# Performance work log

Hardware: AMD Instinct MI355X
Metric: run time of the kernel (lower is better)

The kernel has to match this reference:

```python
import jax, jax.numpy as jnp
import numpy as np

N = 2097152
RES = 512
N_LEVELS = 6  # 512,256,128,64,32,16 (stop at LIGHT_MIN_RES=16)
MIN_ROUGHNESS = 0.08
MAX_ROUGHNESS = 0.5


def _dot(a, b):
    return jnp.sum(a * b, axis=-1, keepdims=True)


def _safe_normalize(x):
    return x / jnp.sqrt(jnp.clip(_dot(x, x), 1e-20, None))


def _reflect(x, n):
    return 2.0 * _dot(x, n) * n - x


def _rgb_to_srgb(x):
    return jnp.where(x <= 0.0031308, 12.92 * x,
                     1.055 * jnp.power(jnp.maximum(x, 0.0031308), 1.0 / 2.4) - 0.055)


def _cube_face_uv(d):
    # OpenGL / nvdiffrast cube-map convention (inverse of util.cube_to_dir)
    x, y, z = d[..., 0], d[..., 1], d[..., 2]
    ax, ay, az = jnp.abs(x), jnp.abs(y), jnp.abs(z)
    is_x = (ax >= ay) & (ax >= az)
    is_y = (~is_x) & (ay >= az)
    face = jnp.where(is_x, jnp.where(x > 0, 0, 1),
           jnp.where(is_y, jnp.where(y > 0, 2, 3),
                           jnp.where(z > 0, 4, 5)))
    ma = jnp.maximum(jnp.where(is_x, ax, jnp.where(is_y, ay, az)), 1e-20)
    u = jnp.where(is_x, jnp.where(x > 0, -z, z),
        jnp.where(is_y, x, jnp.where(z > 0, x, -x)))
    v = jnp.where(is_y, jnp.where(y > 0, z, -z), -y)
    return face, u / ma, v / ma


def _bilinear_gather(tex, face, fx, fy):
    # tex: [6,H,W,C]; face/fx/fy: [N]
    H, W = tex.shape[1], tex.shape[2]
    x0 = jnp.floor(fx); y0 = jnp.floor(fy)
    tx = (fx - x0)[:, None]; ty = (fy - y0)[:, None]
    x0i = jnp.clip(x0.astype(jnp.int32), 0, W - 1)
    x1i = jnp.clip(x0i + 1, 0, W - 1)
    y0i = jnp.clip(y0.astype(jnp.int32), 0, H - 1)
    y1i = jnp.clip(y0i + 1, 0, H - 1)
    c00 = tex[face, y0i, x0i]; c01 = tex[face, y0i, x1i]
    c10 = tex[face, y1i, x0i]; c11 = tex[face, y1i, x1i]
    return (c00 * (1 - tx) + c01 * tx) * (1 - ty) + (c10 * (1 - tx) + c11 * tx) * ty


def _sample_cubemap(tex, dirs):
    H, W = tex.shape[1], tex.shape[2]
    face, u, v = _cube_face_uv(dirs)
    return _bilinear_gather(tex, face, (u * 0.5 + 0.5) * W - 0.5, (v * 0.5 + 0.5) * H - 0.5)


def _sample_cubemap_mip(mips, dirs, level):
    # trilinear: bilinear in each of the two bracketing mip levels + lerp on level
    L = len(mips)
    samples = jnp.stack([_sample_cubemap(m, dirs) for m in mips], axis=0)  # [L,N,C]
    lvl = jnp.clip(level, 0.0, L - 1.0)
    l0 = jnp.floor(lvl).astype(jnp.int32)
    l1 = jnp.minimum(l0 + 1, L - 1)
    f = (lvl - l0.astype(lvl.dtype))[:, None]
    n = jnp.arange(dirs.shape[0])
    return samples[l0, n] * (1 - f) + samples[l1, n] * f


def _sample_lut(lut, uv):
    # lut: [H,W,C]; uv in [0,1], u -> width, v -> height, clamp boundary
    H, W = lut.shape[0], lut.shape[1]
    fx = uv[:, 0] * W - 0.5; fy = uv[:, 1] * H - 0.5
    x0 = jnp.floor(fx); y0 = jnp.floor(fy)
    tx = (fx - x0)[:, None]; ty = (fy - y0)[:, None]
    x0i = jnp.clip(x0.astype(jnp.int32), 0, W - 1); x1i = jnp.clip(x0i + 1, 0, W - 1)
    y0i = jnp.clip(y0.astype(jnp.int32), 0, H - 1); y1i = jnp.clip(y0i + 1, 0, H - 1)
    c00 = lut[y0i, x0i]; c01 = lut[y0i, x1i]; c10 = lut[y1i, x0i]; c11 = lut[y1i, x1i]
    return (c00 * (1 - tx) + c01 * tx) * (1 - ty) + (c10 * (1 - tx) + c11 * tx) * ty


def _get_mip(roughness, n_levels):
    lo = (jnp.clip(roughness, MIN_ROUGHNESS, MAX_ROUGHNESS) - MIN_ROUGHNESS) \
         / (MAX_ROUGHNESS - MIN_ROUGHNESS) * (n_levels - 2)
    hi = (jnp.clip(roughness, MAX_ROUGHNESS, 1.0) - MAX_ROUGHNESS) / (1.0 - MAX_ROUGHNESS) + n_levels - 2
    return jnp.where(roughness < MAX_ROUGHNESS, lo, hi)


def _shade(view_dir, normal, kd, ks, reflect_occ, diffuse_map, mips, fg_lut):
    roughness = ks[:, 1:2]
    metallic = ks[:, 2:3]
    spec_col = (1.0 - metallic) * 0.04 + kd * metallic
    diff_col = kd * (1.0 - metallic)
    reflvec = _safe_normalize(_reflect(view_dir, normal))
    diffuse = jnp.clip(_sample_cubemap(diffuse_map, normal), 0.0, None)
    shaded = diffuse * diff_col * (1.0 - ks[:, 0:1])
    NdotV = jnp.clip(_dot(view_dir, normal), 1e-4, None)
    fg = _sample_lut(fg_lut, jnp.concatenate([NdotV, roughness], axis=-1))
    miplevel = _get_mip(roughness[:, 0], len(mips))
    spec = jnp.clip(_sample_cubemap_mip(mips, reflvec, miplevel), 0.0, None)
    reflectance = spec_col * fg[:, 0:1] + fg[:, 1:2]
    shaded = shaded + spec * reflectance * (1.0 - reflect_occ)
    return _rgb_to_srgb(jnp.clip(shaded, 0.0, 1.0))


def setup_inputs() -> dict:
    key = jax.random.key(0)
    k = jax.random.split(key, 16)
    inp = {
        "view_dir": _safe_normalize(jax.random.normal(k[0], (N, 3), jnp.float32)),
        "normal": _safe_normalize(jax.random.normal(k[1], (N, 3), jnp.float32)),
        "kd": jax.random.uniform(k[2], (N, 3), jnp.float32),
        "ks": jax.random.uniform(k[3], (N, 3), jnp.float32),
        "reflect_occ": jax.random.uniform(k[4], (N, 1), jnp.float32),
    }
    # learned / prefiltered environment light parameters (from build_mips)
    inp["diffuse_map"] = jax.random.uniform(k[5], (6, 16, 16, 3), jnp.float32)
    res = RES
    for i in range(N_LEVELS):
        inp[f"spec{i}"] = jax.random.uniform(k[6 + i], (6, res, res, 3), jnp.float32)
        res //= 2
    inp["fg_lut"] = jax.random.uniform(k[12], (256, 256, 2), jnp.float32)
    return inp


def reference(view_dir, normal, kd, ks, reflect_occ, diffuse_map,
              spec0, spec1, spec2, spec3, spec4, spec5, fg_lut):
    mips = [spec0, spec1, spec2, spec3, spec4, spec5]
    return _shade(view_dir, normal, kd, ks, reflect_occ, diffuse_map, mips, fg_lut)
```

## Files before the change

kernel.cpp:

```cpp
#include <hip/hip_runtime.h>
#include <hip/hip_fp16.h>
#include <math.h>


typedef unsigned int u32;

__device__ __forceinline__ u32 enc9e5(float r, float g, float b) {
    r = fminf(fmaxf(r, 0.f), 65408.f);
    g = fminf(fmaxf(g, 0.f), 65408.f);
    b = fminf(fmaxf(b, 0.f), 65408.f);
    float maxc = fmaxf(r, fmaxf(g, b));
    int e = ((__float_as_int(maxc) >> 23) & 0xff) - 127;
    int exp_p = max(e + 16, 0);
    float denom = __int_as_float((exp_p + 103) << 23);
    int maxm = (int)(maxc / denom + 0.5f);
    if (maxm == 512) { exp_p += 1; denom *= 2.f; }
    float rd = 1.f / denom;
    u32 rm = (u32)(r * rd + 0.5f);
    u32 gm = (u32)(g * rd + 0.5f);
    u32 bm = (u32)(b * rd + 0.5f);
    return rm | (gm << 9) | (bm << 18) | ((u32)exp_p << 27);
}

__device__ __forceinline__ void dec9e5_acc(u32 pk, float w, float& r, float& g, float& b) {
    float scale = __int_as_float((int)(((pk >> 27) & 31u) + 103u) << 23) * w;
    r += (float)(pk & 511u) * scale;
    g += (float)((pk >> 9) & 511u) * scale;
    b += (float)((pk >> 18) & 511u) * scale;
}

struct CubeQ { int idx; float w00, w01, w10, w11; };

__device__ __forceinline__ CubeQ cube_addr_q(int lr, float dx, float dy, float dz) {
    float ax = fabsf(dx), ay = fabsf(dy), az = fabsf(dz);
    bool is_x = (ax >= ay) && (ax >= az);
    bool is_y = (!is_x) && (ay >= az);
    int face = is_x ? (dx > 0.f ? 0 : 1)
                    : (is_y ? (dy > 0.f ? 2 : 3) : (dz > 0.f ? 4 : 5));
    float ma = fmaxf(is_x ? ax : (is_y ? ay : az), 1e-20f);
    float u = is_x ? (dx > 0.f ? -dz : dz) : (is_y ? dx : (dz > 0.f ? dx : -dx));
    float v = is_y ? (dy > 0.f ? dz : -dz) : -dy;
    float inv = __builtin_amdgcn_rcpf(ma);
    float R = (float)(1 << lr);
    float fx = (u * inv * 0.5f + 0.5f) * R - 0.5f;
    float fy = (v * inv * 0.5f + 0.5f) * R - 0.5f;
    float x0f = floorf(fx), y0f = floorf(fy);
    float tx = fx - x0f, ty = fy - y0f;
    int W = 1 << lr;
    int x0 = min(max((int)x0f, 0), W - 1);
    int y0 = min(max((int)y0f, 0), W - 1);
    CubeQ a;
    a.idx = (face << (2 * lr)) + (y0 << lr) + x0;
    a.w00 = (1.f - tx) * (1.f - ty);
    a.w01 = tx * (1.f - ty);
    a.w10 = (1.f - tx) * ty;
    a.w11 = tx * ty;
    return a;
}

__device__ __forceinline__ void gather_q9(uint4 q, const CubeQ& a,
                                          float& r, float& g, float& b) {
    r = 0.f; g = 0.f; b = 0.f;
    dec9e5_acc(q.x, a.w00, r, g, b);
    dec9e5_acc(q.y, a.w01, r, g, b);
    dec9e5_acc(q.z, a.w10, r, g, b);
    dec9e5_acc(q.w, a.w11, r, g, b);
}

__device__ __forceinline__ float srgb1(float x) {
    float p = 1.055f * __builtin_amdgcn_exp2f(
                  __builtin_amdgcn_logf(fmaxf(x, 0.0031308f)) * (1.0f / 2.4f)) - 0.055f;
    return (x <= 0.0031308f) ? (12.92f * x) : p;
}

#define SPEC_TOTAL 2096640
#define DIF_OFF    SPEC_TOTAL
#define LUT_OFF    (SPEC_TOTAL + 1536)
#define ALL_QUADS  (SPEC_TOTAL + 1536 + 65536)

__global__ __launch_bounds__(256)
void repack_all(const float* __restrict__ s0, const float* __restrict__ s1,
                const float* __restrict__ s2, const float* __restrict__ s3,
                const float* __restrict__ s4, const float* __restrict__ s5,
                const float* __restrict__ diffuse_map,
                const float2* __restrict__ lut,
                uint4* __restrict__ dst)
{
    int i = blockIdx.x * blockDim.x + threadIdx.x;
    if (i >= ALL_QUADS) return;

    if (i >= LUT_OFF) {
        int k = i - LUT_OFF;
        int y = k >> 8, x = k & 255;
        int x1 = min(x + 1, 255), y1 = min(y + 1, 255);
        float2 c00 = lut[(y << 8) + x],  c01 = lut[(y << 8) + x1];
        float2 c10 = lut[(y1 << 8) + x], c11 = lut[(y1 << 8) + x1];
        __half2 h00 = __floats2half2_rn(c00.x, c00.y);
        __half2 h01 = __floats2half2_rn(c01.x, c01.y);
        __half2 h10 = __floats2half2_rn(c10.x, c10.y);
        __half2 h11 = __floats2half2_rn(c11.x, c11.y);
        uint4 q;
        q.x = *reinterpret_cast<u32*>(&h00);
        q.y = *reinterpret_cast<u32*>(&h01);
        q.z = *reinterpret_cast<u32*>(&h10);
        q.w = *reinterpret_cast<u32*>(&h11);
        dst[i] = q;
        return;
    }

    const float* src;
    int lr, local;
    if (i >= DIF_OFF)       { src = diffuse_map; lr = 4; local = i - DIF_OFF; }
    else if (i < 1572864)   { src = s0; lr = 9; local = i; }
    else if (i < 1966080)   { src = s1; lr = 8; local = i - 1572864; }
    else if (i < 2064384)   { src = s2; lr = 7; local = i - 1966080; }
    else if (i < 2088960)   { src = s3; lr = 6; local = i - 2064384; }
    else if (i < 2095104)   { src = s4; lr = 5; local = i - 2088960; }
    else                    { src = s5; lr = 4; local = i - 2095104; }

    int W = 1 << lr;
    int face = local >> (2 * lr);
    int rem = local & (W * W - 1);
    int y = rem >> lr, x = rem & (W - 1);
    int x1 = min(x + 1, W - 1), y1 = min(y + 1, W - 1);
    int base = face << (2 * lr);
    int i00 = 3 * (base + (y << lr) + x);
    int i01 = 3 * (base + (y << lr) + x1);
    int i10 = 3 * (base + (y1 << lr) + x);
    int i11 = 3 * (base + (y1 << lr) + x1);
    uint4 q;
    q.x = enc9e5(src[i00], src[i00 + 1], src[i00 + 2]);
    q.y = enc9e5(src[i01], src[i01 + 1], src[i01 + 2]);
    q.z = enc9e5(src[i10], src[i10 + 1], src[i10 + 2]);
    q.w = enc9e5(src[i11], src[i11 + 1], src[i11 + 2]);
    dst[i] = q;
}

struct MipSel { const uint4* tA; const uint4* tB; float f; };

__device__ __forceinline__ MipSel mip_select(const uint4* __restrict__ q, float rough) {
    const float MINR = 0.08f, MAXR = 0.5f;
    float lo = (fminf(fmaxf(rough, MINR), MAXR) - MINR) * (4.0f / (MAXR - MINR));
    float hi = (fminf(fmaxf(rough, MAXR), 1.0f) - MAXR) * (1.0f / (1.0f - MAXR)) + 4.0f;
    float lvl = (rough < MAXR) ? lo : hi;
    lvl = fminf(fmaxf(lvl, 0.f), 5.f);
    int l0 = min(max((int)floorf(lvl), 0), 5);
    int l1 = min(l0 + 1, 5);
    static const int OFF[6] = {0, 1572864, 1966080, 2064384, 2088960, 2095104};
    MipSel s;
    s.tA = q + OFF[l0];
    s.tB = q + OFF[l1];
    s.f = lvl - (float)l0;
    return s;
}

__global__ __launch_bounds__(256)
void envlight_quad4(const float4* __restrict__ vd4,
                    const float4* __restrict__ nm4,
                    const float4* __restrict__ kd4,
                    const float4* __restrict__ ks4,
                    const float4* __restrict__ oc4,
                    const uint4* __restrict__ q,
                    float4* __restrict__ out4, int n4)
{
    int t = blockIdx.x * blockDim.x + threadIdx.x;
    if (t >= n4) return;

    float vf[12], nf[12], kf[12], qf[12], of[12];
    *(float4*)&vf[0] = vd4[3 * t];     *(float4*)&vf[4] = vd4[3 * t + 1];  *(float4*)&vf[8] = vd4[3 * t + 2];
    *(float4*)&nf[0] = nm4[3 * t];     *(float4*)&nf[4] = nm4[3 * t + 1];  *(float4*)&nf[8] = nm4[3 * t + 2];
    *(float4*)&kf[0] = kd4[3 * t];     *(float4*)&kf[4] = kd4[3 * t + 1];  *(float4*)&kf[8] = kd4[3 * t + 2];
    *(float4*)&qf[0] = ks4[3 * t];     *(float4*)&qf[4] = ks4[3 * t + 1];  *(float4*)&qf[8] = ks4[3 * t + 2];
    float4 occ4 = oc4[t];
    float occv[4] = {occ4.x, occ4.y, occ4.z, occ4.w};

    const uint4* dquad = q + DIF_OFF;
    const uint4* lutq  = q + LUT_OFF;

    CubeQ aA[4], aB[4], aD[4];
    int lutI[4];
    float lw00[4], lw01[4], lw10[4], lw11[4];
    float fmip[4], vdotn_[4];
    const uint4 *pA[4], *pB[4];

    #pragma unroll
    for (int p = 0; p < 4; ++p) {
        float vx = vf[3 * p], vy = vf[3 * p + 1], vz = vf[3 * p + 2];
        float nx = nf[3 * p], ny = nf[3 * p + 1], nz = nf[3 * p + 2];
        float rough = qf[3 * p + 1];

        float vdotn = vx * nx + vy * ny + vz * nz;
        vdotn_[p] = vdotn;
        float rx = 2.f * vdotn * nx - vx;
        float ry = 2.f * vdotn * ny - vy;
        float rz = 2.f * vdotn * nz - vz;
        float rlen2 = fmaxf(rx * rx + ry * ry + rz * rz, 1e-20f);
        float rinv = __builtin_amdgcn_rsqf(rlen2);
        rx *= rinv; ry *= rinv; rz *= rinv;

        aD[p] = cube_addr_q(4, nx, ny, nz);

        float NdotV = fmaxf(vdotn, 1e-4f);
        float fx = NdotV * 256.f - 0.5f;
        float fy = rough * 256.f - 0.5f;
        float x0f = floorf(fx), y0f = floorf(fy);
        float tx = fx - x0f, ty = fy - y0f;
        int x0 = min(max((int)x0f, 0), 255);
        int y0 = min(max((int)y0f, 0), 255);
        lutI[p] = (y0 << 8) + x0;
        lw00[p] = (1.f - tx) * (1.f - ty);
        lw01[p] = tx * (1.f - ty);
        lw10[p] = (1.f - tx) * ty;
        lw11[p] = tx * ty;

        MipSel ms = mip_select(q, rough);
        fmip[p] = ms.f;
        pA[p] = ms.tA; pB[p] = ms.tB;
        const float MINR = 0.08f, MAXR = 0.5f;
        float lo = (fminf(fmaxf(rough, MINR), MAXR) - MINR) * (4.0f / (MAXR - MINR));
        float hi = (fminf(fmaxf(rough, MAXR), 1.0f) - MAXR) * (1.0f / (1.0f - MAXR)) + 4.0f;
        float lvl = (rough < MAXR) ? lo : hi;
        lvl = fminf(fmaxf(lvl, 0.f), 5.f);
        int l0 = min(max((int)floorf(lvl), 0), 5);
        int l1 = min(l0 + 1, 5);
        aA[p] = cube_addr_q(9 - l0, rx, ry, rz);
        aB[p] = cube_addr_q(9 - l1, rx, ry, rz);
    }

    uint4 qA[4], qB[4], lq[4], dq[4];
    #pragma unroll
    for (int p = 0; p < 4; ++p) {
        qA[p] = pA[p][aA[p].idx];
        qB[p] = pB[p][aB[p].idx];
        lq[p] = lutq[lutI[p]];
        dq[p] = dquad[aD[p].idx];
    }

    #pragma unroll
    for (int p = 0; p < 4; ++p) {
        float kdx = kf[3 * p], kdy = kf[3 * p + 1], kdz = kf[3 * p + 2];
        float ks0 = qf[3 * p], metallic = qf[3 * p + 2];

        float ar, ag, ab_, br, bg, bb;
        gather_q9(qA[p], aA[p], ar, ag, ab_);
        gather_q9(qB[p], aB[p], br, bg, bb);

        __half2 h00 = *reinterpret_cast<__half2*>(&lq[p].x);
        __half2 h01 = *reinterpret_cast<__half2*>(&lq[p].y);
        __half2 h10 = *reinterpret_cast<__half2*>(&lq[p].z);
        __half2 h11 = *reinterpret_cast<__half2*>(&lq[p].w);
        float2 c00 = __half22float2(h00), c01 = __half22float2(h01);
        float2 c10 = __half22float2(h10), c11 = __half22float2(h11);
        float fg0 = c00.x * lw00[p] + c01.x * lw01[p] + c10.x * lw10[p] + c11.x * lw11[p];
        float fg1 = c00.y * lw00[p] + c01.y * lw01[p] + c10.y * lw10[p] + c11.y * lw11[p];

        float dfr, dfg, dfb;
        gather_q9(dq[p], aD[p], dfr, dfg, dfb);
        dfr = fmaxf(dfr, 0.f); dfg = fmaxf(dfg, 0.f); dfb = fmaxf(dfb, 0.f);

        float f = fmip[p];
        float spr = fmaxf(ar * (1.f - f) + br * f, 0.f);
        float spg = fmaxf(ag * (1.f - f) + bg * f, 0.f);
        float spb = fmaxf(ab_ * (1.f - f) + bb * f, 0.f);

        float m = metallic;
        float scx = (1.f - m) * 0.04f + kdx * m;
        float scy = (1.f - m) * 0.04f + kdy * m;
        float scz = (1.f - m) * 0.04f + kdz * m;
        float dcx = kdx * (1.f - m);
        float dcy = kdy * (1.f - m);
        float dcz = kdz * (1.f - m);

        float kds = 1.f - ks0;
        float shx = dfr * dcx * kds;
        float shy = dfg * dcy * kds;
        float shz = dfb * dcz * kds;

        float om = 1.f - occv[p];
        shx += spr * (scx * fg0 + fg1) * om;
        shy += spg * (scy * fg0 + fg1) * om;
        shz += spb * (scz * fg0 + fg1) * om;

        of[3 * p + 0] = srgb1(fminf(fmaxf(shx, 0.f), 1.f));
        of[3 * p + 1] = srgb1(fminf(fmaxf(shy, 0.f), 1.f));
        of[3 * p + 2] = srgb1(fminf(fmaxf(shz, 0.f), 1.f));
    }

    out4[3 * t]     = *(float4*)&of[0];
    out4[3 * t + 1] = *(float4*)&of[4];
    out4[3 * t + 2] = *(float4*)&of[8];
}

__global__ __launch_bounds__(256)
void envlight_quad1(const float* __restrict__ view_dir,
                    const float* __restrict__ normal,
                    const float* __restrict__ kd,
                    const float* __restrict__ ks,
                    const float* __restrict__ reflect_occ,
                    const uint4* __restrict__ q,
                    float* __restrict__ out, int base, int n)
{
    int i = base + blockIdx.x * blockDim.x + threadIdx.x;
    if (i >= n) return;

    const uint4* dquad = q + DIF_OFF;
    const uint4* lutq  = q + LUT_OFF;

    float vx = view_dir[3 * i + 0], vy = view_dir[3 * i + 1], vz = view_dir[3 * i + 2];
    float nx = normal[3 * i + 0],  ny = normal[3 * i + 1],  nz = normal[3 * i + 2];
    float kdx = kd[3 * i + 0], kdy = kd[3 * i + 1], kdz = kd[3 * i + 2];
    float ks0 = ks[3 * i + 0], rough = ks[3 * i + 1], metallic = ks[3 * i + 2];
    float occ = reflect_occ[i];

    float vdotn = vx * nx + vy * ny + vz * nz;
    float rx = 2.f * vdotn * nx - vx;
    float ry = 2.f * vdotn * ny - vy;
    float rz = 2.f * vdotn * nz - vz;
    float rlen2 = fmaxf(rx * rx + ry * ry + rz * rz, 1e-20f);
    float rinv = __builtin_amdgcn_rsqf(rlen2);
    rx *= rinv; ry *= rinv; rz *= rinv;

    CubeQ aD = cube_addr_q(4, nx, ny, nz);

    float NdotV = fmaxf(vdotn, 1e-4f);
    float fx = NdotV * 256.f - 0.5f;
    float fy = rough * 256.f - 0.5f;
    float x0f = floorf(fx), y0f = floorf(fy);
    float tx = fx - x0f, ty = fy - y0f;
    int x0 = min(max((int)x0f, 0), 255);
    int y0 = min(max((int)y0f, 0), 255);
    int lutI = (y0 << 8) + x0;
    float lw00 = (1.f - tx) * (1.f - ty);
    float lw01 = tx * (1.f - ty);
    float lw10 = (1.f - tx) * ty;
    float lw11 = tx * ty;

    const float MINR = 0.08f, MAXR = 0.5f;
    float lo = (fminf(fmaxf(rough, MINR), MAXR) - MINR) * (4.0f / (MAXR - MINR));
    float hi = (fminf(fmaxf(rough, MAXR), 1.0f) - MAXR) * (1.0f / (1.0f - MAXR)) + 4.0f;
    float lvl = (rough < MAXR) ? lo : hi;
    lvl = fminf(fmaxf(lvl, 0.f), 5.f);
    int l0 = min(max((int)floorf(lvl), 0), 5);
    int l1 = min(l0 + 1, 5);
    float f = lvl - (float)l0;
    static const int OFF[6] = {0, 1572864, 1966080, 2064384, 2088960, 2095104};
    const uint4* tA = q + OFF[l0];
    const uint4* tB = q + OFF[l1];
    CubeQ aA = cube_addr_q(9 - l0, rx, ry, rz);
    CubeQ aB = cube_addr_q(9 - l1, rx, ry, rz);

    uint4 qA = tA[aA.idx];
    uint4 qB = tB[aB.idx];
    uint4 lq = lutq[lutI];
    uint4 dq = dquad[aD.idx];

    float ar, ag, ab_, br, bg, bb;
    gather_q9(qA, aA, ar, ag, ab_);
    gather_q9(qB, aB, br, bg, bb);

    __half2 h00 = *reinterpret_cast<__half2*>(&lq.x);
    __half2 h01 = *reinterpret_cast<__half2*>(&lq.y);
    __half2 h10 = *reinterpret_cast<__half2*>(&lq.z);
    __half2 h11 = *reinterpret_cast<__half2*>(&lq.w);
    float2 c00 = __half22float2(h00), c01 = __half22float2(h01);
    float2 c10 = __half22float2(h10), c11 = __half22float2(h11);
    float fg0 = c00.x * lw00 + c01.x * lw01 + c10.x * lw10 + c11.x * lw11;
    float fg1 = c00.y * lw00 + c01.y * lw01 + c10.y * lw10 + c11.y * lw11;

    float dfr, dfg, dfb;
    gather_q9(dq, aD, dfr, dfg, dfb);
    dfr = fmaxf(dfr, 0.f); dfg = fmaxf(dfg, 0.f); dfb = fmaxf(dfb, 0.f);

    float spr = fmaxf(ar * (1.f - f) + br * f, 0.f);
    float spg = fmaxf(ag * (1.f - f) + bg * f, 0.f);
    float spb = fmaxf(ab_ * (1.f - f) + bb * f, 0.f);

    float m = metallic;
    float scx = (1.f - m) * 0.04f + kdx * m;
    float scy = (1.f - m) * 0.04f + kdy * m;
    float scz = (1.f - m) * 0.04f + kdz * m;
    float dcx = kdx * (1.f - m);
    float dcy = kdy * (1.f - m);
    float dcz = kdz * (1.f - m);

    float kds = 1.f - ks0;
    float shx = dfr * dcx * kds;
    float shy = dfg * dcy * kds;
    float shz = dfb * dcz * kds;

    float om = 1.f - occ;
    shx += spr * (scx * fg0 + fg1) * om;
    shy += spg * (scy * fg0 + fg1) * om;
    shz += spb * (scz * fg0 + fg1) * om;

    out[3 * i + 0] = srgb1(fminf(fmaxf(shx, 0.f), 1.f));
    out[3 * i + 1] = srgb1(fminf(fmaxf(shy, 0.f), 1.f));
    out[3 * i + 2] = srgb1(fminf(fmaxf(shz, 0.f), 1.f));
}

extern "C" void kernel_launch(void* const* d_in, const int* in_sizes, int n_in,
                              void* d_out, int out_size, void* d_ws, size_t ws_size,
                              hipStream_t stream) {
    const float* view_dir    = (const float*)d_in[0];
    const float* normal      = (const float*)d_in[1];
    const float* kd          = (const float*)d_in[2];
    const float* ks          = (const float*)d_in[3];
    const float* reflect_occ = (const float*)d_in[4];
    const float* diffuse_map = (const float*)d_in[5];
    const float* s0          = (const float*)d_in[6];
    const float* s1          = (const float*)d_in[7];
    const float* s2          = (const float*)d_in[8];
    const float* s3          = (const float*)d_in[9];
    const float* s4          = (const float*)d_in[10];
    const float* s5          = (const float*)d_in[11];
    const float* fg_lut      = (const float*)d_in[12];
    float* out = (float*)d_out;

    int n = in_sizes[0] / 3;
    const size_t NEED_Q = (size_t)ALL_QUADS * 16;

    if (ws_size >= NEED_Q) {
        uint4* q = (uint4*)d_ws;
        repack_all<<<(ALL_QUADS + 255) / 256, 256, 0, stream>>>(
            s0, s1, s2, s3, s4, s5, diffuse_map, (const float2*)fg_lut, q);

        int n4 = n / 4;
        if (n4 > 0) {
            envlight_quad4<<<(n4 + 255) / 256, 256, 0, stream>>>(
                (const float4*)view_dir, (const float4*)normal,
                (const float4*)kd, (const float4*)ks,
                (const float4*)reflect_occ, q, (float4*)out, n4);
        }
        int tail = n - 4 * n4;
        if (tail > 0) {
            envlight_quad1<<<1, 256, 0, stream>>>(
                view_dir, normal, kd, ks, reflect_occ, q, out, 4 * n4, n);
        }
    } else {
        int n4 = n / 4;
        envlight_quad4<<<(n4 + 255) / 256, 256, 0, stream>>>(
            (const float4*)view_dir, (const float4*)normal,
            (const float4*)kd, (const float4*)ks,
            (const float4*)reflect_occ, (const uint4*)d_ws, (float4*)out, n4);
    }
}
```

Baseline: 226.6 us.

## Replace 4-pixel-per-thread shading kernel with one-pixel-per-thread kernel

Drops the float4-vectorised kernel that shaded four pixels per thread and uses a scalar kernel that shades one pixel per thread, with launch bounds asking for 8 blocks per SM. The second mip level's coordinates are now derived from the first level's by halving instead of rerunning the cube face projection. The aim is lower register pressure and higher occupancy so more gathers are in flight, at the cost of losing 16-byte vector loads and stores on the streaming inputs. A fallback kernel that samples the raw float textures is added for when the workspace is too small, fixing the old path that read an unfilled workspace.

Result: slower. 235.9 us (+4.1%).

```diff
diff --git a/kernel.cpp b/kernel.cpp
--- a/kernel.cpp
+++ b/kernel.cpp
@@ -29,48 +29,38 @@
     b += (float)((pk >> 18) & 511u) * scale;
 }
 
-struct CubeQ { int idx; float w00, w01, w10, w11; };
-
-__device__ __forceinline__ CubeQ cube_addr_q(int lr, float dx, float dy, float dz) {
-    float ax = fabsf(dx), ay = fabsf(dy), az = fabsf(dz);
-    bool is_x = (ax >= ay) && (ax >= az);
-    bool is_y = (!is_x) && (ay >= az);
-    int face = is_x ? (dx > 0.f ? 0 : 1)
-                    : (is_y ? (dy > 0.f ? 2 : 3) : (dz > 0.f ? 4 : 5));
-    float ma = fmaxf(is_x ? ax : (is_y ? ay : az), 1e-20f);
-    float u = is_x ? (dx > 0.f ? -dz : dz) : (is_y ? dx : (dz > 0.f ? dx : -dx));
-    float v = is_y ? (dy > 0.f ? dz : -dz) : -dy;
-    float inv = __builtin_amdgcn_rcpf(ma);
-    float R = (float)(1 << lr);
-    float fx = (u * inv * 0.5f + 0.5f) * R - 0.5f;
-    float fy = (v * inv * 0.5f + 0.5f) * R - 0.5f;
-    float x0f = floorf(fx), y0f = floorf(fy);
-    float tx = fx - x0f, ty = fy - y0f;
-    int W = 1 << lr;
-    int x0 = min(max((int)x0f, 0), W - 1);
-    int y0 = min(max((int)y0f, 0), W - 1);
-    CubeQ a;
-    a.idx = (face << (2 * lr)) + (y0 << lr) + x0;
-    a.w00 = (1.f - tx) * (1.f - ty);
-    a.w01 = tx * (1.f - ty);
-    a.w10 = (1.f - tx) * ty;
-    a.w11 = tx * ty;
-    return a;
-}
-
-__device__ __forceinline__ void gather_q9(uint4 q, const CubeQ& a,
+__device__ __forceinline__ void gather_q9(uint4 q, float tx, float ty,
                                           float& r, float& g, float& b) {
+    float w01 = tx * (1.f - ty);
+    float w00 = (1.f - tx) * (1.f - ty);
+    float w10 = (1.f - tx) * ty;
+    float w11 = tx * ty;
     r = 0.f; g = 0.f; b = 0.f;
-    dec9e5_acc(q.x, a.w00, r, g, b);
-    dec9e5_acc(q.y, a.w01, r, g, b);
-    dec9e5_acc(q.z, a.w10, r, g, b);
-    dec9e5_acc(q.w, a.w11, r, g, b);
+    dec9e5_acc(q.x, w00, r, g, b);
+    dec9e5_acc(q.y, w01, r, g, b);
+    dec9e5_acc(q.z, w10, r, g, b);
+    dec9e5_acc(q.w, w11, r, g, b);
 }
 
 __device__ __forceinline__ float srgb1(float x) {
     float p = 1.055f * __builtin_amdgcn_exp2f(
                   __builtin_amdgcn_logf(fmaxf(x, 0.0031308f)) * (1.0f / 2.4f)) - 0.055f;
     return (x <= 0.0031308f) ? (12.92f * x) : p;
+}
+
+__device__ __forceinline__ void cube_face_uv(float dx, float dy, float dz,
+                                             int& face, float& u, float& v) {
+    float ax = fabsf(dx), ay = fabsf(dy), az = fabsf(dz);
+    bool is_x = (ax >= ay) && (ax >= az);
+    bool is_y = (!is_x) && (ay >= az);
+    face = is_x ? (dx > 0.f ? 0 : 1)
+                : (is_y ? (dy > 0.f ? 2 : 3) : (dz > 0.f ? 4 : 5));
+    float ma = fmaxf(is_x ? ax : (is_y ? ay : az), 1e-20f);
+    float uu = is_x ? (dx > 0.f ? -dz : dz) : (is_y ? dx : (dz > 0.f ? dx : -dx));
+    float vv = is_y ? (dy > 0.f ? dz : -dz) : -dy;
+    float inv = __builtin_amdgcn_rcpf(ma);
+    u = uu * inv;
+    v = vv * inv;
 }
 
 #define SPEC_TOTAL 2096640
@@ -136,9 +126,55 @@
     dst[i] = q;
 }
 
-struct MipSel { const uint4* tA; const uint4* tB; float f; };
-
-__device__ __forceinline__ MipSel mip_select(const uint4* __restrict__ q, float rough) {
+__global__ __launch_bounds__(256, 8)
+void envlight_q1(const float* __restrict__ view_dir,
+                 const float* __restrict__ normal,
+                 const float* __restrict__ kd,
+                 const float* __restrict__ ks,
+                 const float* __restrict__ reflect_occ,
+                 const uint4* __restrict__ q,
+                 float* __restrict__ out, int n)
+{
+    int i = blockIdx.x * blockDim.x + threadIdx.x;
+    if (i >= n) return;
+
+    float vx = view_dir[3 * i + 0], vy = view_dir[3 * i + 1], vz = view_dir[3 * i + 2];
+    float nx = normal[3 * i + 0],  ny = normal[3 * i + 1],  nz = normal[3 * i + 2];
+    float rough = ks[3 * i + 1];
+
+    float vdotn = vx * nx + vy * ny + vz * nz;
+    float rx = 2.f * vdotn * nx - vx;
+    float ry = 2.f * vdotn * ny - vy;
+    float rz = 2.f * vdotn * nz - vz;
+    float rlen2 = fmaxf(rx * rx + ry * ry + rz * rz, 1e-20f);
+    float rinv = __builtin_amdgcn_rsqf(rlen2);
+    rx *= rinv; ry *= rinv; rz *= rinv;
+
+    float dtx, dty; int dIdx;
+    {
+        int face; float u, v;
+        cube_face_uv(nx, ny, nz, face, u, v);
+        float fx = (u * 0.5f + 0.5f) * 16.f - 0.5f;
+        float fy = (v * 0.5f + 0.5f) * 16.f - 0.5f;
+        float x0f = floorf(fx), y0f = floorf(fy);
+        dtx = fx - x0f; dty = fy - y0f;
+        int x0 = min(max((int)x0f, 0), 15);
+        int y0 = min(max((int)y0f, 0), 15);
+        dIdx = (face << 8) + (y0 << 4) + x0;
+    }
+
+    float ltx, lty; int lutI;
+    {
+        float NdotV = fmaxf(vdotn, 1e-4f);
+        float fx = NdotV * 256.f - 0.5f;
+        float fy = rough * 256.f - 0.5f;
+        float x0f = floorf(fx), y0f = floorf(fy);
+        ltx = fx - x0f; lty = fy - y0f;
+        int x0 = min(max((int)x0f, 0), 255);
+        int y0 = min(max((int)y0f, 0), 255);
+        lutI = (y0 << 8) + x0;
+    }
+
     const float MINR = 0.08f, MAXR = 0.5f;
     float lo = (fminf(fmaxf(rough, MINR), MAXR) - MINR) * (4.0f / (MAXR - MINR));
     float hi = (fminf(fmaxf(rough, MAXR), 1.0f) - MAXR) * (1.0f / (1.0f - MAXR)) + 4.0f;
@@ -146,217 +182,50 @@
     lvl = fminf(fmaxf(lvl, 0.f), 5.f);
     int l0 = min(max((int)floorf(lvl), 0), 5);
     int l1 = min(l0 + 1, 5);
-    static const int OFF[6] = {0, 1572864, 1966080, 2064384, 2088960, 2095104};
-    MipSel s;
-    s.tA = q + OFF[l0];
-    s.tB = q + OFF[l1];
-    s.f = lvl - (float)l0;
-    return s;
-}
-
-__global__ __launch_bounds__(256)
-void envlight_quad4(const float4* __restrict__ vd4,
-                    const float4* __restrict__ nm4,
-                    const float4* __restrict__ kd4,
-                    const float4* __restrict__ ks4,
-                    const float4* __restrict__ oc4,
-                    const uint4* __restrict__ q,
-                    float4* __restrict__ out4, int n4)
-{
-    int t = blockIdx.x * blockDim.x + threadIdx.x;
-    if (t >= n4) return;
-
-    float vf[12], nf[12], kf[12], qf[12], of[12];
-    *(float4*)&vf[0] = vd4[3 * t];     *(float4*)&vf[4] = vd4[3 * t + 1];  *(float4*)&vf[8] = vd4[3 * t + 2];
-    *(float4*)&nf[0] = nm4[3 * t];     *(float4*)&nf[4] = nm4[3 * t + 1];  *(float4*)&nf[8] = nm4[3 * t + 2];
-    *(float4*)&kf[0] = kd4[3 * t];     *(float4*)&kf[4] = kd4[3 * t + 1];  *(float4*)&kf[8] = kd4[3 * t + 2];
-    *(float4*)&qf[0] = ks4[3 * t];     *(float4*)&qf[4] = ks4[3 * t + 1];  *(float4*)&qf[8] = ks4[3 * t + 2];
-    float4 occ4 = oc4[t];
-    float occv[4] = {occ4.x, occ4.y, occ4.z, occ4.w};
-
-    const uint4* dquad = q + DIF_OFF;
-    const uint4* lutq  = q + LUT_OFF;
-
-    CubeQ aA[4], aB[4], aD[4];
-    int lutI[4];
-    float lw00[4], lw01[4], lw10[4], lw11[4];
-    float fmip[4], vdotn_[4];
-    const uint4 *pA[4], *pB[4];
-
-    #pragma unroll
-    for (int p = 0; p < 4; ++p) {
-        float vx = vf[3 * p], vy = vf[3 * p + 1], vz = vf[3 * p + 2];
-        float nx = nf[3 * p], ny = nf[3 * p + 1], nz = nf[3 * p + 2];
-        float rough = qf[3 * p + 1];
-
-        float vdotn = vx * nx + vy * ny + vz * nz;
-        vdotn_[p] = vdotn;
-        float rx = 2.f * vdotn * nx - vx;
-        float ry = 2.f * vdotn * ny - vy;
-        float rz = 2.f * vdotn * nz - vz;
-        float rlen2 = fmaxf(rx * rx + ry * ry + rz * rz, 1e-20f);
-        float rinv = __builtin_amdgcn_rsqf(rlen2);
-        rx *= rinv; ry *= rinv; rz *= rinv;
-
-        aD[p] = cube_addr_q(4, nx, ny, nz);
-
-        float NdotV = fmaxf(vdotn, 1e-4f);
-        float fx = NdotV * 256.f - 0.5f;
-        float fy = rough * 256.f - 0.5f;
-        float x0f = floorf(fx), y0f = floorf(fy);
-        float tx = fx - x0f, ty = fy - y0f;
-        int x0 = min(max((int)x0f, 0), 255);
-        int y0 = min(max((int)y0f, 0), 255);
-        lutI[p] = (y0 << 8) + x0;
-        lw00[p] = (1.f - tx) * (1.f - ty);
-        lw01[p] = tx * (1.f - ty);
-        lw10[p] = (1.f - tx) * ty;
-        lw11[p] = tx * ty;
-
-        MipSel ms = mip_select(q, rough);
-        fmip[p] = ms.f;
-        pA[p] = ms.tA; pB[p] = ms.tB;
-        const float MINR = 0.08f, MAXR = 0.5f;
-        float lo = (fminf(fmaxf(rough, MINR), MAXR) - MINR) * (4.0f / (MAXR - MINR));
-        float hi = (fminf(fmaxf(rough, MAXR), 1.0f) - MAXR) * (1.0f / (1.0f - MAXR)) + 4.0f;
-        float lvl = (rough < MAXR) ? lo : hi;
-        lvl = fminf(fmaxf(lvl, 0.f), 5.f);
-        int l0 = min(max((int)floorf(lvl), 0), 5);
-        int l1 = min(l0 + 1, 5);
-        aA[p] = cube_addr_q(9 - l0, rx, ry, rz);
-        aB[p] = cube_addr_q(9 - l1, rx, ry, rz);
-    }
-
-    uint4 qA[4], qB[4], lq[4], dq[4];
-    #pragma unroll
-    for (int p = 0; p < 4; ++p) {
-        qA[p] = pA[p][aA[p].idx];
-        qB[p] = pB[p][aB[p].idx];
-        lq[p] = lutq[lutI[p]];
-        dq[p] = dquad[aD[p].idx];
-    }
-
-    #pragma unroll
-    for (int p = 0; p < 4; ++p) {
-        float kdx = kf[3 * p], kdy = kf[3 * p + 1], kdz = kf[3 * p + 2];
-        float ks0 = qf[3 * p], metallic = qf[3 * p + 2];
-
-        float ar, ag, ab_, br, bg, bb;
-        gather_q9(qA[p], aA[p], ar, ag, ab_);
-        gather_q9(qB[p], aB[p], br, bg, bb);
-
-        __half2 h00 = *reinterpret_cast<__half2*>(&lq[p].x);
-        __half2 h01 = *reinterpret_cast<__half2*>(&lq[p].y);
-        __half2 h10 = *reinterpret_cast<__half2*>(&lq[p].z);
-        __half2 h11 = *reinterpret_cast<__half2*>(&lq[p].w);
-        float2 c00 = __half22float2(h00), c01 = __half22float2(h01);
-        float2 c10 = __half22float2(h10), c11 = __half22float2(h11);
-        float fg0 = c00.x * lw00[p] + c01.x * lw01[p] + c10.x * lw10[p] + c11.x * lw11[p];
-        float fg1 = c00.y * lw00[p] + c01.y * lw01[p] + c10.y * lw10[p] + c11.y * lw11[p];
-
-        float dfr, dfg, dfb;
-        gather_q9(dq[p], aD[p], dfr, dfg, dfb);
-        dfr = fmaxf(dfr, 0.f); dfg = fmaxf(dfg, 0.f); dfb = fmaxf(dfb, 0.f);
-
-        float f = fmip[p];
-        float spr = fmaxf(ar * (1.f - f) + br * f, 0.f);
-        float spg = fmaxf(ag * (1.f - f) + bg * f, 0.f);
-        float spb = fmaxf(ab_ * (1.f - f) + bb * f, 0.f);
-
-        float m = metallic;
-        float scx = (1.f - m) * 0.04f + kdx * m;
-        float scy = (1.f - m) * 0.04f + kdy * m;
-        float scz = (1.f - m) * 0.04f + kdz * m;
-        float dcx = kdx * (1.f - m);
-        float dcy = kdy * (1.f - m);
-        float dcz = kdz * (1.f - m);
-
-        float kds = 1.f - ks0;
-        float shx = dfr * dcx * kds;
-        float shy = dfg * dcy * kds;
-        float shz = dfb * dcz * kds;
-
-        float om = 1.f - occv[p];
-        shx += spr * (scx * fg0 + fg1) * om;
-        shy += spg * (scy * fg0 + fg1) * om;
-        shz += spb * (scz * fg0 + fg1) * om;
-
-        of[3 * p + 0] = srgb1(fminf(fmaxf(shx, 0.f), 1.f));
-        of[3 * p + 1] = srgb1(fminf(fmaxf(shy, 0.f), 1.f));
-        of[3 * p + 2] = srgb1(fminf(fmaxf(shz, 0.f), 1.f));
-    }
-
-    out4[3 * t]     = *(float4*)&of[0];
-    out4[3 * t + 1] = *(float4*)&of[4];
-    out4[3 * t + 2] = *(float4*)&of[8];
-}
-
-__global__ __launch_bounds__(256)
-void envlight_quad1(const float* __restrict__ view_dir,
-                    const float* __restrict__ normal,
-                    const float* __restrict__ kd,
-                    const float* __restrict__ ks,
-                    const float* __restrict__ reflect_occ,
-                    const uint4* __restrict__ q,
-                    float* __restrict__ out, int base, int n)
-{
-    int i = base + blockIdx.x * blockDim.x + threadIdx.x;
-    if (i >= n) return;
-
-    const uint4* dquad = q + DIF_OFF;
-    const uint4* lutq  = q + LUT_OFF;
-
-    float vx = view_dir[3 * i + 0], vy = view_dir[3 * i + 1], vz = view_dir[3 * i + 2];
-    float nx = normal[3 * i + 0],  ny = normal[3 * i + 1],  nz = normal[3 * i + 2];
-    float kdx = kd[3 * i + 0], kdy = kd[3 * i + 1], kdz = kd[3 * i + 2];
-    float ks0 = ks[3 * i + 0], rough = ks[3 * i + 1], metallic = ks[3 * i + 2];
-    float occ = reflect_occ[i];
-
-    float vdotn = vx * nx + vy * ny + vz * nz;
-    float rx = 2.f * vdotn * nx - vx;
-    float ry = 2.f * vdotn * ny - vy;
-    float rz = 2.f * vdotn * nz - vz;
-    float rlen2 = fmaxf(rx * rx + ry * ry + rz * rz, 1e-20f);
-    float rinv = __builtin_amdgcn_rsqf(rlen2);
-    rx *= rinv; ry *= rinv; rz *= rinv;
-
-    CubeQ aD = cube_addr_q(4, nx, ny, nz);
-
-    float NdotV = fmaxf(vdotn, 1e-4f);
-    float fx = NdotV * 256.f - 0.5f;
-    float fy = rough * 256.f - 0.5f;
-    float x0f = floorf(fx), y0f = floorf(fy);
-    float tx = fx - x0f, ty = fy - y0f;
-    int x0 = min(max((int)x0f, 0), 255);
-    int y0 = min(max((int)y0f, 0), 255);
-    int lutI = (y0 << 8) + x0;
-    float lw00 = (1.f - tx) * (1.f - ty);
-    float lw01 = tx * (1.f - ty);
-    float lw10 = (1.f - tx) * ty;
-    float lw11 = tx * ty;
-
-    const float MINR = 0.08f, MAXR = 0.5f;
-    float lo = (fminf(fmaxf(rough, MINR), MAXR) - MINR) * (4.0f / (MAXR - MINR));
-    float hi = (fminf(fmaxf(rough, MAXR), 1.0f) - MAXR) * (1.0f / (1.0f - MAXR)) + 4.0f;
-    float lvl = (rough < MAXR) ? lo : hi;
-    lvl = fminf(fmaxf(lvl, 0.f), 5.f);
-    int l0 = min(max((int)floorf(lvl), 0), 5);
-    int l1 = min(l0 + 1, 5);
-    float f = lvl - (float)l0;
+    float fmip = lvl - (float)l0;
+
+    float atx, aty, btx, bty; int aIdx, bIdx;
+    {
+        int face; float u, v;
+        cube_face_uv(rx, ry, rz, face, u, v);
+        int lrA = 9 - l0, lrB = 9 - l1;
+        float RA = (float)(1 << lrA);
+        float fxA = (u * 0.5f + 0.5f) * RA - 0.5f;
+        float fyA = (v * 0.5f + 0.5f) * RA - 0.5f;
+        float fxB = (l0 == l1) ? fxA : (fxA + 0.5f) * 0.5f - 0.5f;
+        float fyB = (l0 == l1) ? fyA : (fyA + 0.5f) * 0.5f - 0.5f;
+
+        float x0fA = floorf(fxA), y0fA = floorf(fyA);
+        atx = fxA - x0fA; aty = fyA - y0fA;
+        int WA = 1 << lrA;
+        int x0A = min(max((int)x0fA, 0), WA - 1);
+        int y0A = min(max((int)y0fA, 0), WA - 1);
+        aIdx = (face << (2 * lrA)) + (y0A << lrA) + x0A;
+
+        float x0fB = floorf(fxB), y0fB = floorf(fyB);
+        btx = fxB - x0fB; bty = fyB - y0fB;
+        int WB = 1 << lrB;
+        int x0B = min(max((int)x0fB, 0), WB - 1);
+        int y0B = min(max((int)y0fB, 0), WB - 1);
+        bIdx = (face << (2 * lrB)) + (y0B << lrB) + x0B;
+    }
+
     static const int OFF[6] = {0, 1572864, 1966080, 2064384, 2088960, 2095104};
     const uint4* tA = q + OFF[l0];
     const uint4* tB = q + OFF[l1];
-    CubeQ aA = cube_addr_q(9 - l0, rx, ry, rz);
-    CubeQ aB = cube_addr_q(9 - l1, rx, ry, rz);
-
-    uint4 qA = tA[aA.idx];
-    uint4 qB = tB[aB.idx];
-    uint4 lq = lutq[lutI];
-    uint4 dq = dquad[aD.idx];
+
+    uint4 qA = tA[aIdx];
+    uint4 qB = tB[bIdx];
+    uint4 lq = (q + LUT_OFF)[lutI];
+    uint4 dq = (q + DIF_OFF)[dIdx];
+
+    float kdx = kd[3 * i + 0], kdy = kd[3 * i + 1], kdz = kd[3 * i + 2];
+    float ks0 = ks[3 * i + 0], metallic = ks[3 * i + 2];
+    float occ = reflect_occ[i];
 
     float ar, ag, ab_, br, bg, bb;
-    gather_q9(qA, aA, ar, ag, ab_);
-    gather_q9(qB, aB, br, bg, bb);
+    gather_q9(qA, atx, aty, ar, ag, ab_);
+    gather_q9(qB, btx, bty, br, bg, bb);
 
     __half2 h00 = *reinterpret_cast<__half2*>(&lq.x);
     __half2 h01 = *reinterpret_cast<__half2*>(&lq.y);
@@ -364,16 +233,20 @@
     __half2 h11 = *reinterpret_cast<__half2*>(&lq.w);
     float2 c00 = __half22float2(h00), c01 = __half22float2(h01);
     float2 c10 = __half22float2(h10), c11 = __half22float2(h11);
+    float lw00 = (1.f - ltx) * (1.f - lty);
+    float lw01 = ltx * (1.f - lty);
+    float lw10 = (1.f - ltx) * lty;
+    float lw11 = ltx * lty;
     float fg0 = c00.x * lw00 + c01.x * lw01 + c10.x * lw10 + c11.x * lw11;
     float fg1 = c00.y * lw00 + c01.y * lw01 + c10.y * lw10 + c11.y * lw11;
 
     float dfr, dfg, dfb;
-    gather_q9(dq, aD, dfr, dfg, dfb);
+    gather_q9(dq, dtx, dty, dfr, dfg, dfb);
     dfr = fmaxf(dfr, 0.f); dfg = fmaxf(dfg, 0.f); dfb = fmaxf(dfb, 0.f);
 
-    float spr = fmaxf(ar * (1.f - f) + br * f, 0.f);
-    float spg = fmaxf(ag * (1.f - f) + bg * f, 0.f);
-    float spb = fmaxf(ab_ * (1.f - f) + bb * f, 0.f);
+    float spr = fmaxf(ar * (1.f - fmip) + br * fmip, 0.f);
+    float spg = fmaxf(ag * (1.f - fmip) + bg * fmip, 0.f);
+    float spb = fmaxf(ab_ * (1.f - fmip) + bb * fmip, 0.f);
 
     float m = metallic;
     float scx = (1.f - m) * 0.04f + kdx * m;
@@ -392,6 +265,109 @@
     shx += spr * (scx * fg0 + fg1) * om;
     shy += spg * (scy * fg0 + fg1) * om;
     shz += spb * (scz * fg0 + fg1) * om;
+
+    out[3 * i + 0] = srgb1(fminf(fmaxf(shx, 0.f), 1.f));
+    out[3 * i + 1] = srgb1(fminf(fmaxf(shy, 0.f), 1.f));
+    out[3 * i + 2] = srgb1(fminf(fmaxf(shz, 0.f), 1.f));
+}
+
+__global__ __launch_bounds__(256)
+void envlight_raw(const float* __restrict__ view_dir,
+                  const float* __restrict__ normal,
+                  const float* __restrict__ kd,
+                  const float* __restrict__ ks,
+                  const float* __restrict__ reflect_occ,
+                  const float* __restrict__ diffuse_map,
+                  const float* __restrict__ s0, const float* __restrict__ s1,
+                  const float* __restrict__ s2, const float* __restrict__ s3,
+                  const float* __restrict__ s4, const float* __restrict__ s5,
+                  const float* __restrict__ fg_lut,
+                  float* __restrict__ out, int n)
+{
+    int i = blockIdx.x * blockDim.x + threadIdx.x;
+    if (i >= n) return;
+
+    float vx = view_dir[3 * i], vy = view_dir[3 * i + 1], vz = view_dir[3 * i + 2];
+    float nx = normal[3 * i],  ny = normal[3 * i + 1],  nz = normal[3 * i + 2];
+    float kdx = kd[3 * i], kdy = kd[3 * i + 1], kdz = kd[3 * i + 2];
+    float ks0 = ks[3 * i], rough = ks[3 * i + 1], metallic = ks[3 * i + 2];
+    float occ = reflect_occ[i];
+
+    float vdotn = vx * nx + vy * ny + vz * nz;
+    float rx = 2.f * vdotn * nx - vx;
+    float ry = 2.f * vdotn * ny - vy;
+    float rz = 2.f * vdotn * nz - vz;
+    float rinv = __builtin_amdgcn_rsqf(fmaxf(rx * rx + ry * ry + rz * rz, 1e-20f));
+    rx *= rinv; ry *= rinv; rz *= rinv;
+
+    const float* mips[6] = {s0, s1, s2, s3, s4, s5};
+
+    const float MINR = 0.08f, MAXR = 0.5f;
+    float lo = (fminf(fmaxf(rough, MINR), MAXR) - MINR) * (4.0f / (MAXR - MINR));
+    float hi = (fminf(fmaxf(rough, MAXR), 1.0f) - MAXR) * (1.0f / (1.0f - MAXR)) + 4.0f;
+    float lvl = fminf(fmaxf((rough < MAXR) ? lo : hi, 0.f), 5.f);
+    int l0 = min(max((int)floorf(lvl), 0), 5);
+    int l1 = min(l0 + 1, 5);
+    float f = lvl - (float)l0;
+
+    float acc[3][3];
+    float dirs[3][3] = {{nx, ny, nz}, {rx, ry, rz}, {rx, ry, rz}};
+    int lrs[3] = {4, 9 - l0, 9 - l1};
+    const float* texs[3] = {diffuse_map, mips[l0], mips[l1]};
+    for (int s = 0; s < 3; ++s) {
+        int face; float u, v;
+        cube_face_uv(dirs[s][0], dirs[s][1], dirs[s][2], face, u, v);
+        int lr = lrs[s], W = 1 << lr;
+        float fx = (u * 0.5f + 0.5f) * (float)W - 0.5f;
+        float fy = (v * 0.5f + 0.5f) * (float)W - 0.5f;
+        float x0f = floorf(fx), y0f = floorf(fy);
+        float tx = fx - x0f, ty = fy - y0f;
+        int x0 = min(max((int)x0f, 0), W - 1);
+        int x1 = min(x0 + 1, W - 1);
+        int y0 = min(max((int)y0f, 0), W - 1);
+        int y1 = min(y0 + 1, W - 1);
+        int base = face << (2 * lr);
+        const float* t = texs[s];
+        const float* p00 = t + 3 * (base + (y0 << lr) + x0);
+        const float* p01 = t + 3 * (base + (y0 << lr) + x1);
+        const float* p10 = t + 3 * (base + (y1 << lr) + x0);
+        const float* p11 = t + 3 * (base + (y1 << lr) + x1);
+        float w00 = (1.f - tx) * (1.f - ty), w01 = tx * (1.f - ty);
+        float w10 = (1.f - tx) * ty, w11 = tx * ty;
+        for (int c = 0; c < 3; ++c)
+            acc[s][c] = p00[c] * w00 + p01[c] * w01 + p10[c] * w10 + p11[c] * w11;
+    }
+
+    float NdotV = fmaxf(vdotn, 1e-4f);
+    float fx = NdotV * 256.f - 0.5f, fy = rough * 256.f - 0.5f;
+    float x0f = floorf(fx), y0f = floorf(fy);
+    float tx = fx - x0f, ty = fy - y0f;
+    int x0 = min(max((int)x0f, 0), 255);
+    int x1 = min(x0 + 1, 255);
+    int y0 = min(max((int)y0f, 0), 255);
+    int y1 = min(y0 + 1, 255);
+    const float2* lut2 = (const float2*)fg_lut;
+    float2 c00 = lut2[(y0 << 8) + x0], c01 = lut2[(y0 << 8) + x1];
+    float2 c10 = lut2[(y1 << 8) + x0], c11 = lut2[(y1 << 8) + x1];
+    float w00 = (1.f - tx) * (1.f - ty), w01 = tx * (1.f - ty);
+    float w10 = (1.f - tx) * ty, w11 = tx * ty;
+    float fg0 = c00.x * w00 + c01.x * w01 + c10.x * w10 + c11.x * w11;
+    float fg1 = c00.y * w00 + c01.y * w01 + c10.y * w10 + c11.y * w11;
+
+    float dfr = fmaxf(acc[0][0], 0.f), dfg = fmaxf(acc[0][1], 0.f), dfb = fmaxf(acc[0][2], 0.f);
+    float spr = fmaxf(acc[1][0] * (1.f - f) + acc[2][0] * f, 0.f);
+    float spg = fmaxf(acc[1][1] * (1.f - f) + acc[2][1] * f, 0.f);
+    float spb = fmaxf(acc[1][2] * (1.f - f) + acc[2][2] * f, 0.f);
+
+    float m = metallic;
+    float scx = (1.f - m) * 0.04f + kdx * m;
+    float scy = (1.f - m) * 0.04f + kdy * m;
+    float scz = (1.f - m) * 0.04f + kdz * m;
+    float kds = 1.f - ks0;
+    float om = 1.f - occ;
+    float shx = dfr * kdx * (1.f - m) * kds + spr * (scx * fg0 + fg1) * om;
+    float shy = dfg * kdy * (1.f - m) * kds + spg * (scy * fg0 + fg1) * om;
+    float shz = dfb * kdz * (1.f - m) * kds + spb * (scz * fg0 + fg1) * om;
 
     out[3 * i + 0] = srgb1(fminf(fmaxf(shx, 0.f), 1.f));
     out[3 * i + 1] = srgb1(fminf(fmaxf(shy, 0.f), 1.f));
@@ -417,30 +393,19 @@
     float* out = (float*)d_out;
 
     int n = in_sizes[0] / 3;
+    int block = 256;
+    int grid = (n + block - 1) / block;
     const size_t NEED_Q = (size_t)ALL_QUADS * 16;
 
     if (ws_size >= NEED_Q) {
         uint4* q = (uint4*)d_ws;
         repack_all<<<(ALL_QUADS + 255) / 256, 256, 0, stream>>>(
             s0, s1, s2, s3, s4, s5, diffuse_map, (const float2*)fg_lut, q);
-
-        int n4 = n / 4;
-        if (n4 > 0) {
-            envlight_quad4<<<(n4 + 255) / 256, 256, 0, stream>>>(
-                (const float4*)view_dir, (const float4*)normal,
-                (const float4*)kd, (const float4*)ks,
-                (const float4*)reflect_occ, q, (float4*)out, n4);
-        }
-        int tail = n - 4 * n4;
-        if (tail > 0) {
-            envlight_quad1<<<1, 256, 0, stream>>>(
-                view_dir, normal, kd, ks, reflect_occ, q, out, 4 * n4, n);
-        }
+        envlight_q1<<<grid, block, 0, stream>>>(
+            view_dir, normal, kd, ks, reflect_occ, q, out, n);
     } else {
-        int n4 = n / 4;
-        envlight_quad4<<<(n4 + 255) / 256, 256, 0, stream>>>(
-            (const float4*)view_dir, (const float4*)normal,
-            (const float4*)kd, (const float4*)ks,
-            (const float4*)reflect_occ, (const uint4*)d_ws, (float4*)out, n4);
-    }
-}
+        envlight_raw<<<grid, block, 0, stream>>>(
+            view_dir, normal, kd, ks, reflect_occ, diffuse_map,
+            s0, s1, s2, s3, s4, s5, fg_lut, out, n);
+    }
+}
```
